# Performance work log

Measured on AMD Instinct MI355X. Metric: run time of the kernel, lower is better.

The kernel has to match this reference:

```python
import jax, jax.numpy as jnp
import numpy as np

HEADS = 8
DIM_HEAD = 64
SCALE = DIM_HEAD ** -0.5


def entmax15(z, axis=-1):
    """Exact 1.5-entmax via the sort-based algorithm (Peters & Martins 2019)."""
    z = z / 2.0
    z = z - jnp.max(z, axis=axis, keepdims=True)  # shift-invariant, for stability
    zs = -jnp.sort(-z, axis=axis)  # descending
    n = z.shape[axis]
    k = jnp.arange(1, n + 1, dtype=z.dtype)
    mean = jnp.cumsum(zs, axis=axis) / k
    mean_sq = jnp.cumsum(zs * zs, axis=axis) / k
    ss = k * (mean_sq - mean * mean)
    delta = (1.0 - ss) / k
    tau = mean - jnp.sqrt(jnp.maximum(delta, 0.0))
    support = (tau <= zs).astype(jnp.int32)
    k_star = jnp.sum(support, axis=axis, keepdims=True)  # support size >= 1
    tau_star = jnp.take_along_axis(tau, k_star - 1, axis=axis)
    return jnp.square(jnp.maximum(z - tau_star, 0.0))


def setup_inputs() -> dict:
    key = jax.random.key(0)
    k1, k2, k3 = jax.random.split(key, 3)
    b, n, dim = 4, 1024, 512
    inner = HEADS * DIM_HEAD  # 512
    x = jax.random.normal(k1, (b, n, dim), dtype=jnp.float32)
    w_qkv = jax.random.normal(k2, (dim, inner * 3), dtype=jnp.float32) * 0.02
    w_out = jax.random.normal(k3, (inner, dim), dtype=jnp.float32) * 0.02
    return {"x": x, "w_qkv": w_qkv, "w_out": w_out}


def reference(x, w_qkv, w_out):
    b, n, dim = x.shape
    h, d = HEADS, DIM_HEAD
    qkv = x @ w_qkv  # [b, n, 3*h*d]
    q, k, v = jnp.split(qkv, 3, axis=-1)
    # [b, n, h*d] -> [b, h, n, d]
    def to_heads(t):
        return t.reshape(b, n, h, d).transpose(0, 2, 1, 3)
    q, k, v = to_heads(q) * SCALE, to_heads(k), to_heads(v)
    sim = jnp.einsum('bhid,bhjd->bhij', q, k)  # [b, h, n, n]
    attn = entmax15(sim, axis=-1)
    out = jnp.einsum('bhij,bhjd->bhid', attn, v)  # [b, h, n, d]
    out = out.transpose(0, 2, 1, 3).reshape(b, n, h * d)
    return out @ w_out
```

## Files before the change

kernel.cpp:

```cpp
#include <hip/hip_runtime.h>
#include <stdint.h>
#include <stddef.h>


typedef __attribute__((ext_vector_type(4))) float f32x4;
typedef __attribute__((ext_vector_type(2))) float f32x2;
typedef __attribute__((ext_vector_type(8))) short bf16x8;
typedef __attribute__((ext_vector_type(4))) uint32_t u32x4;
typedef __attribute__((ext_vector_type(2))) uint32_t u32x2;

__device__ inline unsigned short f2bf(float f) {
    union { float f; uint32_t u; } cv; cv.f = f;
    uint32_t u = cv.u;
    return (unsigned short)((u + 0x7fffu + ((u >> 16) & 1u)) >> 16);
}
__device__ inline uint32_t packbf2(float lo, float hi) {
    uint32_t r;
    asm("v_cvt_pk_bf16_f32 %0, %1, %2" : "=v"(r) : "v"(lo), "v"(hi));
    return r;
}
__device__ inline void gl_lds16(const short* g, short* l) {
    __builtin_amdgcn_global_load_lds(
        (const __attribute__((address_space(1))) void*)g,
        (__attribute__((address_space(3))) void*)l, 16, 0, 0);
}
__device__ inline f32x2 vmax2(f32x2 a, f32x2 b) { return __builtin_elementwise_max(a, b); }
__device__ inline f32x2 vfma2(f32x2 a, f32x2 b, f32x2 c) { return __builtin_elementwise_fma(a, b, c); }

__global__ __launch_bounds__(256) void convert_all(const float* __restrict__ x,
                                                   const float* __restrict__ wqkv,
                                                   const float* __restrict__ wout,
                                                   short* __restrict__ xb,
                                                   short* __restrict__ wqkvt,
                                                   short* __restrict__ woutt) {
    __shared__ float tl[32][33];
    const int bid = blockIdx.x;
    const int t = threadIdx.x;
    if (bid < 1024) {
        int base = bid * 2048 + t * 8;
        f32x4 v0 = *(const f32x4*)(x + base);
        f32x4 v1 = *(const f32x4*)(x + base + 4);
        u32x4 o = {packbf2(v0[0], v0[1]), packbf2(v0[2], v0[3]),
                   packbf2(v1[0], v1[1]), packbf2(v1[2], v1[3])};
        *(u32x4*)(xb + base) = o;
        return;
    }
    const float* src; short* dst; int NC, tn, tk;
    if (bid < 1024 + 768) {
        int idx = bid - 1024; tn = idx % 48; tk = idx / 48; src = wqkv; dst = wqkvt; NC = 1536;
    } else {
        int idx = bid - 1792; tn = idx % 16; tk = idx / 16; src = wout; dst = woutt; NC = 512;
    }
    const int row = t >> 3, c4 = (t & 7) * 4;
    f32x4 v = *(const f32x4*)(src + (size_t)(tk * 32 + row) * NC + tn * 32 + c4);
    tl[row][c4 + 0] = v[0]; tl[row][c4 + 1] = v[1];
    tl[row][c4 + 2] = v[2]; tl[row][c4 + 3] = v[3];
    __syncthreads();
    float a = tl[c4 + 0][row], b = tl[c4 + 1][row];
    float c = tl[c4 + 2][row], d = tl[c4 + 3][row];
    u32x2 o = {packbf2(a, b), packbf2(c, d)};
    *(u32x2*)(dst + (size_t)(tn * 32 + row) * 512 + tk * 32 + c4) = o;
}

template<int NB, int MODE, int NT>
__global__ __launch_bounds__(256) void gemm_bf16(const short* __restrict__ A,
                                                 const short* __restrict__ Bt,
                                                 void* __restrict__ outp,
                                                 short* __restrict__ vt) {
    constexpr int WN = NT / 2;
    constexpr int NFR = WN / 16;
    __shared__ __align__(16) short As[64 * 32];
    __shared__ __align__(16) short Bs[NT * 32];
    const int t = threadIdx.x;
    const int lane = t & 63;
    const int wv = t >> 6;
    const int quad = lane >> 4;
    const int l16 = lane & 15;
    const int bm = blockIdx.x / NB;
    const int bn = blockIdx.x % NB;
    const int wm = (wv & 1) * 32, wn = (wv >> 1) * WN;

    f32x4 acc[2][NFR];
    #pragma unroll
    for (int i = 0; i < 2; i++)
        #pragma unroll
        for (int j = 0; j < NFR; j++) acc[i][j] = (f32x4){0.f, 0.f, 0.f, 0.f};

    const int sr = t >> 2, sc = (t & 3) * 8;

    for (int kt = 0; kt < 16; kt++) {
        gl_lds16(A + (size_t)(bm * 64 + sr) * 512 + kt * 32 + sc, As + t * 8);
        #pragma unroll
        for (int i = 0; i < NT / 64; i++)
            gl_lds16(Bt + (size_t)(bn * NT + 64 * i + sr) * 512 + kt * 32 + sc,
                     Bs + 64 * i * 32 + t * 8);
        __syncthreads();
        bf16x8 af[2], bfr[NFR];
        #pragma unroll
        for (int mi = 0; mi < 2; mi++)
            af[mi] = *(const bf16x8*)(As + (wm + mi * 16 + l16) * 32 + quad * 8);
        #pragma unroll
        for (int ni = 0; ni < NFR; ni++)
            bfr[ni] = *(const bf16x8*)(Bs + (wn + ni * 16 + l16) * 32 + quad * 8);
        #pragma unroll
        for (int mi = 0; mi < 2; mi++)
            #pragma unroll
            for (int ni = 0; ni < NFR; ni++)
                acc[mi][ni] = __builtin_amdgcn_mfma_f32_16x16x32_bf16(af[mi], bfr[ni], acc[mi][ni], 0, 0, 0);
        __syncthreads();
    }

    if (MODE == 0) {
        short* ob = (short*)outp;
        if (bn < 8) {
            const float scq = (bn < 4) ? 0.0625f : 1.0f;
            #pragma unroll
            for (int mi = 0; mi < 2; mi++)
                #pragma unroll
                for (int ni = 0; ni < NFR; ni++)
                    #pragma unroll
                    for (int rg = 0; rg < 4; rg++)
                        ob[(size_t)(bm * 64 + wm + mi * 16 + quad * 4 + rg) * 1024
                           + bn * NT + wn + ni * 16 + l16] = (short)f2bf(acc[mi][ni][rg] * scq);
        } else {
            #pragma unroll
            for (int mi = 0; mi < 2; mi++) {
                int rowb = bm * 64 + wm + mi * 16 + quad * 4;
                int bbb = rowb >> 10, j = rowb & 1023;
                #pragma unroll
                for (int ni = 0; ni < NFR; ni++) {
                    int vcol = bn * NT + wn + ni * 16 + l16 - 1024;
                    int hh = vcol >> 6, dd = vcol & 63;
                    u32x2 pk = {packbf2(acc[mi][ni][0], acc[mi][ni][1]),
                                packbf2(acc[mi][ni][2], acc[mi][ni][3])};
                    *(u32x2*)(vt + ((size_t)((bbb * 8 + hh) * 64 + dd)) * 1024 + j) = pk;
                }
            }
        }
    } else {
        float* of = (float*)outp;
        #pragma unroll
        for (int mi = 0; mi < 2; mi++)
            #pragma unroll
            for (int ni = 0; ni < NFR; ni++)
                #pragma unroll
                for (int rg = 0; rg < 4; rg++)
                    of[(size_t)(bm * 64 + wm + mi * 16 + quad * 4 + rg) * 512
                       + bn * NT + wn + ni * 16 + l16] = acc[mi][ni][rg];
    }
}

__global__ __launch_bounds__(256, 4) void attn_entmax(const short* __restrict__ qkv,
                                                      const short* __restrict__ vt,
                                                      short* __restrict__ oheads) {
    __shared__ __align__(16) unsigned char smem[32768];
    short* P_lds = (short*)smem;
    float* tbuf = (float*)smem;
    float* osum = (float*)smem;

    const int t = threadIdx.x;
    const int lane = t & 63;
    const int wv = t >> 6;
    const int quad = lane >> 4;
    const int l16 = lane & 15;

    const int xcd = blockIdx.x & 7;
    const int g = blockIdx.x >> 3;
    const int hb = xcd * 4 + (g >> 6);
    const int rt = g & 63;
    const int bb = hb >> 3, hh = hb & 7;
    const int r0 = rt * 16;

    bf16x8 a0, a1;
    {
        const short* qp = qkv + (size_t)(bb * 1024 + r0 + l16) * 1024 + hh * 64 + quad * 8;
        a0 = *(const bf16x8*)qp;
        a1 = *(const bf16x8*)(qp + 32);
    }

    f32x2 zT2[32];
    const short* kb0 = qkv + (size_t)(bb * 1024) * 1024 + 512 + hh * 64 + quad * 8;
    const int rown = quad * 4 + wv;
    for (int ci = 0; ci < 4; ci++) {
        f32x4 zc[4];
        #pragma unroll
        for (int f = 0; f < 4; f++) {
            int supl = f >> 1, jj = f & 1;
            int j0 = (ci * 2 + supl) * 128 + (wv + 4 * jj) * 16 + l16;
            const short* kp = kb0 + (size_t)j0 * 1024;
            bf16x8 b0 = *(const bf16x8*)kp;
            bf16x8 b1 = *(const bf16x8*)(kp + 32);
            f32x4 acc = {0.f, 0.f, 0.f, 0.f};
            acc = __builtin_amdgcn_mfma_f32_16x16x32_bf16(a0, b0, acc, 0, 0, 0);
            acc = __builtin_amdgcn_mfma_f32_16x16x32_bf16(a1, b1, acc, 0, 0, 0);
            zc[f] = acc;
        }
        __syncthreads();
        #pragma unroll
        for (int f = 0; f < 4; f++) {
            int supl = f >> 1, jj = f & 1;
            int colc = supl * 128 + (wv + 4 * jj) * 16 + l16;
            #pragma unroll
            for (int rg = 0; rg < 4; rg++)
                tbuf[(quad * 4 + rg) * 268 + colc] = zc[f][rg];
        }
        __syncthreads();
        #pragma unroll
        for (int i = 0; i < 4; i++) {
            f32x4 v = *(const f32x4*)(tbuf + rown * 268 + i * 64 + l16 * 4);
            zT2[ci * 8 + i * 2 + 0] = (f32x2){v[0], v[1]};
            zT2[ci * 8 + i * 2 + 1] = (f32x2){v[2], v[3]};
        }
    }
    __syncthreads();

    float tau;
    {
        f32x2 m2 = zT2[0], p2 = zT2[0];
        f32x2 q2 = zT2[0] * zT2[0];
        #pragma unroll
        for (int i = 1; i < 32; i++) {
            f32x2 v = zT2[i];
            m2 = vmax2(m2, v);
            p2 = p2 + v;
            q2 = vfma2(v, v, q2);
        }
        float mx = fmaxf(m2[0], m2[1]);
        float s1 = p2[0] + p2[1];
        float s2 = q2[0] + q2[1];
        #pragma unroll
        for (int s = 1; s < 16; s <<= 1) {
            mx = fmaxf(mx, __shfl_xor(mx, s, 64));
            s1 += __shfl_xor(s1, s, 64);
            s2 += __shfl_xor(s2, s, 64);
        }
        float mean = s1 * (1.0f / 1024.0f);
        float disc = fmaxf(mean * mean - (s2 - 1.0f) * (1.0f / 1024.0f), 0.0f);
        tau = mean - __builtin_sqrtf(disc);
        tau = fminf(tau, mx - 0.03125f);
        tau = fmaxf(tau, mx - 1.0f);
    }

    const f32x2 zero2 = {0.f, 0.f};
    #pragma unroll 1
    for (int it = 0; it < 7; it++) {
        f32x2 tau2 = {tau, tau};
        f32x2 s1a = zero2, s1b = zero2, s2a = zero2, s2b = zero2;
        #pragma unroll
        for (int i = 0; i < 16; i++) {
            f32x2 ra = vmax2(zT2[i * 2] - tau2, zero2);
            f32x2 rb = vmax2(zT2[i * 2 + 1] - tau2, zero2);
            s1a = s1a + ra; s1b = s1b + rb;
            s2a = vfma2(ra, ra, s2a); s2b = vfma2(rb, rb, s2b);
        }
        float s1 = (s1a[0] + s1a[1]) + (s1b[0] + s1b[1]);
        float s2 = (s2a[0] + s2a[1]) + (s2b[0] + s2b[1]);
        #pragma unroll
        for (int s = 1; s < 16; s <<= 1) {
            s1 += __shfl_xor(s1, s, 64);
            s2 += __shfl_xor(s2, s, 64);
        }
        tau += (s2 - 1.0f) * 0.5f * __builtin_amdgcn_rcpf(s1);
    }

    {
        const f32x2 tau2 = {tau, tau};
        const int dg = l16;
        const int ra = rown & 7;
        #pragma unroll
        for (int ci = 0; ci < 4; ci++)
            #pragma unroll
            for (int i = 0; i < 4; i++) {
                f32x2 r01 = vmax2(zT2[ci * 8 + i * 2] - tau2, zero2);
                f32x2 r23 = vmax2(zT2[ci * 8 + i * 2 + 1] - tau2, zero2);
                f32x2 p01 = r01 * r01, p23 = r23 * r23;
                u32x2 pk = {packbf2(p01[0], p01[1]), packbf2(p23[0], p23[1])};
                int jb = ci * 32 + i * 8 + (dg >> 1);
                *(u32x2*)(P_lds + rown * 1024 + ((jb ^ ra) << 3) + (dg & 1) * 4) = pk;
            }
    }
    __syncthreads();

    f32x4 oacc[4];
    #pragma unroll
    for (int nt = 0; nt < 4; nt++) oacc[nt] = (f32x4){0.f, 0.f, 0.f, 0.f};
    const short* vb0 = vt + (size_t)((bb * 8 + hh) * 64) * 1024;
    const int lra = l16 & 7;
    #pragma unroll
    for (int sup = 0; sup < 8; sup++) {
        int jb = sup * 16 + wv * 4 + quad;
        bf16x8 pf = *(const bf16x8*)(P_lds + l16 * 1024 + ((jb ^ lra) << 3));
        #pragma unroll
        for (int nt = 0; nt < 4; nt++) {
            bf16x8 bv = *(const bf16x8*)(vb0 + (size_t)(nt * 16 + l16) * 1024
                                         + sup * 128 + wv * 32 + quad * 8);
            oacc[nt] = __builtin_amdgcn_mfma_f32_16x16x32_bf16(pf, bv, oacc[nt], 0, 0, 0);
        }
    }
    __syncthreads();

    #pragma unroll
    for (int nt = 0; nt < 4; nt++)
        #pragma unroll
        for (int rg = 0; rg < 4; rg++)
            osum[(wv * 16 + quad * 4 + rg) * 68 + nt * 16 + l16] = oacc[nt][rg];
    __syncthreads();
    #pragma unroll
    for (int i = 0; i < 2; i++) {
        int idx = t + 256 * i;
        int r = idx >> 5, dp = idx & 31;
        float e0 = 0.f, e1 = 0.f;
        #pragma unroll
        for (int w = 0; w < 4; w++) {
            e0 += osum[(w * 16 + r) * 68 + dp * 2];
            e1 += osum[(w * 16 + r) * 68 + dp * 2 + 1];
        }
        *(uint32_t*)(oheads + (size_t)(bb * 1024 + r0 + r) * 512 + hh * 64 + dp * 2) = packbf2(e0, e1);
    }
}

extern "C" void kernel_launch(void* const* d_in, const int* in_sizes, int n_in,
                              void* d_out, int out_size, void* d_ws, size_t ws_size,
                              hipStream_t stream) {
    (void)in_sizes; (void)n_in; (void)out_size; (void)ws_size;
    const float* x     = (const float*)d_in[0];
    const float* w_qkv = (const float*)d_in[1];
    const float* w_out = (const float*)d_in[2];
    float* out = (float*)d_out;

    char* ws = (char*)d_ws;
    short* qkv_b = (short*)(ws);
    short* vt    = (short*)(ws + 8388608);
    short* ohead = (short*)(ws + 12582912);
    short* xb    = (short*)(ws + 16777216);
    short* wqkvt = (short*)(ws + 20971520);
    short* woutt = (short*)(ws + 22544384);

    convert_all<<<dim3(2048), dim3(256), 0, stream>>>(x, w_qkv, w_out, xb, wqkvt, woutt);
    gemm_bf16<12, 0, 128><<<dim3(64 * 12), dim3(256), 0, stream>>>(xb, wqkvt, (void*)qkv_b, vt);
    attn_entmax<<<dim3(2048), dim3(256), 0, stream>>>(qkv_b, vt, ohead);
    gemm_bf16<8, 1, 64><<<dim3(64 * 8), dim3(256), 0, stream>>>(ohead, woutt, (void*)out, nullptr);
}
```

Baseline: 151.3 us.

## Store K and V in per-head fragment-tiled layouts for coalesced attention loads

```diff
diff --git a/kernel.cpp b/kernel.cpp
--- a/kernel.cpp
+++ b/kernel.cpp
@@ -66,7 +66,8 @@
 __global__ __launch_bounds__(256) void gemm_bf16(const short* __restrict__ A,
                                                  const short* __restrict__ Bt,
                                                  void* __restrict__ outp,
-                                                 short* __restrict__ vt) {
+                                                 short* __restrict__ vt3,
+                                                 short* __restrict__ kh) {
     constexpr int WN = NT / 2;
     constexpr int NFR = WN / 16;
     __shared__ __align__(16) short As[64 * 32];
@@ -111,17 +112,32 @@
     }
 
     if (MODE == 0) {
-        short* ob = (short*)outp;
-        if (bn < 8) {
-            const float scq = (bn < 4) ? 0.0625f : 1.0f;
+        if (bn < 4) {
+            short* ob = (short*)outp;
             #pragma unroll
             for (int mi = 0; mi < 2; mi++)
                 #pragma unroll
                 for (int ni = 0; ni < NFR; ni++)
                     #pragma unroll
                     for (int rg = 0; rg < 4; rg++)
-                        ob[(size_t)(bm * 64 + wm + mi * 16 + quad * 4 + rg) * 1024
-                           + bn * NT + wn + ni * 16 + l16] = (short)f2bf(acc[mi][ni][rg] * scq);
+                        ob[(size_t)(bm * 64 + wm + mi * 16 + quad * 4 + rg) * 512
+                           + bn * NT + wn + ni * 16 + l16] = (short)f2bf(acc[mi][ni][rg] * 0.0625f);
+        } else if (bn < 8) {
+            #pragma unroll
+            for (int mi = 0; mi < 2; mi++) {
+                int rowb = bm * 64 + wm + mi * 16 + quad * 4;
+                int bbb = rowb >> 10, jj0 = rowb & 1023;
+                #pragma unroll
+                for (int ni = 0; ni < NFR; ni++) {
+                    int c = bn * NT + wn + ni * 16 + l16 - 512;
+                    int hh = c >> 6, dh = c & 63;
+                    short* base = kh + (size_t)(bbb * 8 + hh) * 65536
+                                  + (size_t)(jj0 >> 4) * 1024 + (dh >> 3) * 128 + (dh & 7);
+                    #pragma unroll
+                    for (int rg = 0; rg < 4; rg++)
+                        base[((jj0 & 15) + rg) * 8] = (short)f2bf(acc[mi][ni][rg]);
+                }
+            }
         } else {
             #pragma unroll
             for (int mi = 0; mi < 2; mi++) {
@@ -133,7 +149,8 @@
                     int hh = vcol >> 6, dd = vcol & 63;
                     u32x2 pk = {packbf2(acc[mi][ni][0], acc[mi][ni][1]),
                                 packbf2(acc[mi][ni][2], acc[mi][ni][3])};
-                    *(u32x2*)(vt + ((size_t)((bbb * 8 + hh) * 64 + dd)) * 1024 + j) = pk;
+                    *(u32x2*)(vt3 + (size_t)(bbb * 8 + hh) * 65536
+                              + (size_t)(j >> 3) * 512 + dd * 8 + (j & 7)) = pk;
                 }
             }
         }
@@ -150,8 +167,9 @@
     }
 }
 
-__global__ __launch_bounds__(256, 4) void attn_entmax(const short* __restrict__ qkv,
-                                                      const short* __restrict__ vt,
+__global__ __launch_bounds__(256, 4) void attn_entmax(const short* __restrict__ qb,
+                                                      const short* __restrict__ kh,
+                                                      const short* __restrict__ vt3,
                                                       short* __restrict__ oheads) {
     __shared__ __align__(16) unsigned char smem[32768];
     short* P_lds = (short*)smem;
@@ -173,23 +191,25 @@
 
     bf16x8 a0, a1;
     {
-        const short* qp = qkv + (size_t)(bb * 1024 + r0 + l16) * 1024 + hh * 64 + quad * 8;
+        const short* qp = qb + (size_t)(bb * 1024 + r0 + l16) * 512 + hh * 64 + quad * 8;
         a0 = *(const bf16x8*)qp;
         a1 = *(const bf16x8*)(qp + 32);
     }
 
+    const short* khh = kh + (size_t)(bb * 8 + hh) * 65536;
+    const short* vb0 = vt3 + (size_t)(bb * 8 + hh) * 65536;
+
     f32x2 zT2[32];
-    const short* kb0 = qkv + (size_t)(bb * 1024) * 1024 + 512 + hh * 64 + quad * 8;
     const int rown = quad * 4 + wv;
     for (int ci = 0; ci < 4; ci++) {
         f32x4 zc[4];
         #pragma unroll
         for (int f = 0; f < 4; f++) {
             int supl = f >> 1, jj = f & 1;
-            int j0 = (ci * 2 + supl) * 128 + (wv + 4 * jj) * 16 + l16;
-            const short* kp = kb0 + (size_t)j0 * 1024;
-            bf16x8 b0 = *(const bf16x8*)kp;
-            bf16x8 b1 = *(const bf16x8*)(kp + 32);
+            int jtile = (ci * 2 + supl) * 8 + (wv + 4 * jj);
+            const short* kp = khh + (size_t)jtile * 1024 + l16 * 8;
+            bf16x8 b0 = *(const bf16x8*)(kp + quad * 128);
+            bf16x8 b1 = *(const bf16x8*)(kp + (4 + quad) * 128);
             f32x4 acc = {0.f, 0.f, 0.f, 0.f};
             acc = __builtin_amdgcn_mfma_f32_16x16x32_bf16(a0, b0, acc, 0, 0, 0);
             acc = __builtin_amdgcn_mfma_f32_16x16x32_bf16(a1, b1, acc, 0, 0, 0);
@@ -284,16 +304,15 @@
     f32x4 oacc[4];
     #pragma unroll
     for (int nt = 0; nt < 4; nt++) oacc[nt] = (f32x4){0.f, 0.f, 0.f, 0.f};
-    const short* vb0 = vt + (size_t)((bb * 8 + hh) * 64) * 1024;
     const int lra = l16 & 7;
     #pragma unroll
     for (int sup = 0; sup < 8; sup++) {
         int jb = sup * 16 + wv * 4 + quad;
         bf16x8 pf = *(const bf16x8*)(P_lds + l16 * 1024 + ((jb ^ lra) << 3));
+        const short* vs = vb0 + (size_t)jb * 512;
         #pragma unroll
         for (int nt = 0; nt < 4; nt++) {
-            bf16x8 bv = *(const bf16x8*)(vb0 + (size_t)(nt * 16 + l16) * 1024
-                                         + sup * 128 + wv * 32 + quad * 8);
+            bf16x8 bv = *(const bf16x8*)(vs + (nt * 16 + l16) * 8);
             oacc[nt] = __builtin_amdgcn_mfma_f32_16x16x32_bf16(pf, bv, oacc[nt], 0, 0, 0);
         }
     }
@@ -329,15 +348,16 @@
     float* out = (float*)d_out;
 
     char* ws = (char*)d_ws;
-    short* qkv_b = (short*)(ws);
-    short* vt    = (short*)(ws + 8388608);
+    short* qb    = (short*)(ws);
+    short* kh    = (short*)(ws + 4194304);
+    short* vt3   = (short*)(ws + 8388608);
     short* ohead = (short*)(ws + 12582912);
     short* xb    = (short*)(ws + 16777216);
     short* wqkvt = (short*)(ws + 20971520);
     short* woutt = (short*)(ws + 22544384);
 
     convert_all<<<dim3(2048), dim3(256), 0, stream>>>(x, w_qkv, w_out, xb, wqkvt, woutt);
-    gemm_bf16<12, 0, 128><<<dim3(64 * 12), dim3(256), 0, stream>>>(xb, wqkvt, (void*)qkv_b, vt);
-    attn_entmax<<<dim3(2048), dim3(256), 0, stream>>>(qkv_b, vt, ohead);
-    gemm_bf16<8, 1, 64><<<dim3(64 * 8), dim3(256), 0, stream>>>(ohead, woutt, (void*)out, nullptr);
-}
+    gemm_bf16<12, 0, 128><<<dim3(64 * 12), dim3(256), 0, stream>>>(xb, wqkvt, (void*)qb, vt3, kh);
+    attn_entmax<<<dim3(2048), dim3(256), 0, stream>>>(qb, kh, vt3, ohead);
+    gemm_bf16<8, 1, 64><<<dim3(64 * 8), dim3(256), 0, stream>>>(ohead, woutt, (void*)out, nullptr, nullptr);
+}
```

Result: faster. 126.5 us (-16.4%).
